# Kernel optimization log

Hardware: AMD Instinct MI355X
Metric: run time of the kernel (lower is better)

## Reference

```python
import jax, jax.numpy as jnp
import numpy as np

N_NODES = 20000
N_EDGES = 320000
NUM_FEATURES = 128
HIDDEN = 128
NUM_CLASSES = 40
GRID_SIZE = 4
SPLINE_ORDER = 3
NB = GRID_SIZE + SPLINE_ORDER  # basis functions per input feature
_H = 2.0 / GRID_SIZE  # grid_range [-1, 1]
GRID = jnp.arange(-SPLINE_ORDER, GRID_SIZE + SPLINE_ORDER + 1, dtype=jnp.float32) * _H - 1.0


def b_splines(x):
    # x: (N, in) -> (N, in, NB) via Cox-de Boor recursion (efficient-KAN)
    xg = x[..., None]
    b = ((xg >= GRID[:-1]) & (xg < GRID[1:])).astype(x.dtype)
    for k in range(1, SPLINE_ORDER + 1):
        b = ((xg - GRID[: -(k + 1)]) / (GRID[k:-1] - GRID[: -(k + 1)]) * b[..., :-1]
             + (GRID[k + 1:] - xg) / (GRID[k + 1:] - GRID[1:-k]) * b[..., 1:])
    return b


def kan_linear(x, base_w, spline_w):
    # base branch: silu(x) @ W_base^T ; spline branch: contraction over (in, NB)
    base = jax.nn.silu(x) @ base_w.T
    spline = jnp.einsum('nik,oik->no', b_splines(x), spline_w)
    return base + spline


def gcn_conv(h, base_w, spline_w, bias, src_f, dst_f, norm):
    h = kan_linear(h, base_w, spline_w)
    msg = h[src_f] * norm[:, None]  # gather + edge scaling
    out = jax.ops.segment_sum(msg, dst_f, num_segments=N_NODES)
    return out + bias


def batchnorm(h, gamma, beta):
    mean = h.mean(axis=0)
    var = h.var(axis=0)  # biased, as torch BN uses for normalization
    return (h - mean) * jax.lax.rsqrt(var + 1e-5) * gamma + beta


def setup_inputs() -> dict:
    key = jax.random.key(0)
    ks = jax.random.split(key, 8)
    s = 0.1
    return {
        'x': jax.random.normal(ks[0], (N_NODES, NUM_FEATURES), dtype=jnp.float32),
        'edge_index': jax.random.randint(ks[1], (2, N_EDGES), 0, N_NODES, dtype=jnp.int64),
        'base_w0': jax.random.normal(ks[2], (HIDDEN, NUM_FEATURES), dtype=jnp.float32) * s,
        'spline_w0': jax.random.normal(ks[3], (HIDDEN, NUM_FEATURES, NB), dtype=jnp.float32) * s,
        'bias0': jnp.zeros((HIDDEN,), dtype=jnp.float32),
        'base_w1': jax.random.normal(ks[4], (HIDDEN, HIDDEN), dtype=jnp.float32) * s,
        'spline_w1': jax.random.normal(ks[5], (HIDDEN, HIDDEN, NB), dtype=jnp.float32) * s,
        'bias1': jnp.zeros((HIDDEN,), dtype=jnp.float32),
        'base_w_out': jax.random.normal(ks[6], (NUM_CLASSES, NUM_FEATURES + 2 * HIDDEN), dtype=jnp.float32) * s,
        'spline_w_out': jax.random.normal(ks[7], (NUM_CLASSES, NUM_FEATURES + 2 * HIDDEN, NB), dtype=jnp.float32) * s,
        'bias_out': jnp.zeros((NUM_CLASSES,), dtype=jnp.float32),
        'gamma': jnp.ones((HIDDEN,), dtype=jnp.float32),
        'beta': jnp.zeros((HIDDEN,), dtype=jnp.float32),
    }


def reference(x, edge_index, base_w0, spline_w0, bias0, base_w1, spline_w1, bias1,
              base_w_out, spline_w_out, bias_out, gamma, beta):
    # gcn_norm with self loops (computed once, reused by every layer)
    loop = jnp.arange(N_NODES, dtype=edge_index.dtype)
    src_f = jnp.concatenate([edge_index[0], loop])
    dst_f = jnp.concatenate([edge_index[1], loop])
    deg = jax.ops.segment_sum(jnp.ones_like(dst_f, dtype=x.dtype), dst_f, num_segments=N_NODES)
    dinv = jnp.where(deg > 0, jax.lax.rsqrt(jnp.maximum(deg, 1e-12)), 0.0)
    norm = dinv[src_f] * dinv[dst_f]

    skips = [x]
    h = x
    for bw, sw, b in ((base_w0, spline_w0, bias0), (base_w1, spline_w1, bias1)):
        h = gcn_conv(h, bw, sw, b, src_f, dst_f, norm)
        h = batchnorm(h, gamma, beta)  # shared BN, dropout p=0.0 is identity
        skips.append(h)
    h = jnp.concatenate(skips, axis=1)  # (N, 128 + 2*128)
    return gcn_conv(h, base_w_out, spline_w_out, bias_out, src_f, dst_f, norm)
```

## Files before the change

kernel.cpp:

```cpp
#include <hip/hip_runtime.h>

#define NN 20000

typedef _Float16 half8 __attribute__((ext_vector_type(8)));
typedef _Float16 half2v __attribute__((ext_vector_type(2)));
typedef float floatx16 __attribute__((ext_vector_type(16)));

#define MFMA32(a, b, c) __builtin_amdgcn_mfma_f32_32x32x16_f16((a), (b), (c), 0, 0, 0)
#define LD8(p) (*(const half8*)(p))

__device__ __forceinline__ void gl_lds16(const _Float16* g, _Float16* l) {
  __builtin_amdgcn_global_load_lds((const __attribute__((address_space(1))) char*)g,
                                   (__attribute__((address_space(3))) char*)l, 16, 0, 0);
}

__device__ __forceinline__ void bspline7_fast(float x, float b[7]) {
  float u = (x + 2.5f) * 2.0f;
  float cf = floorf(u);
  int c = (int)cf;
  float t = u - cf;
  float omt = 1.0f - t;
  float t2 = t * t, t3 = t2 * t;
  float w0 = omt * omt * omt * (1.0f / 6.0f);
  float w1 = (3.0f * t3 - 6.0f * t2 + 4.0f) * (1.0f / 6.0f);
  float w2 = (-3.0f * t3 + 3.0f * t2 + 3.0f * t + 1.0f) * (1.0f / 6.0f);
  float w3 = t3 * (1.0f / 6.0f);
  bool valid = (c >= 0) && (c <= 9);
#pragma unroll
  for (int i = 0; i < 7; ++i) {
    int d = c - i;
    float w = (d == 0) ? w3 : (d == 1) ? w2 : (d == 2) ? w1 : (d == 3) ? w0 : 0.0f;
    b[i] = valid ? w : 0.0f;
  }
}

__device__ __forceinline__ float silu_f(float x) {
  return x * (1.0f / (1.0f + __expf(-x)));
}

__device__ __forceinline__ half8 afrag(float xv) {
  float b[7];
  bspline7_fast(xv, b);
  half8 hv;
  hv[0] = (_Float16)silu_f(xv);
#pragma unroll
  for (int k = 0; k < 7; ++k) hv[k + 1] = (_Float16)b[k];
  return hv;
}

__global__ void fb_kernel(const float* __restrict__ X, const float* __restrict__ ss,
                          _Float16* __restrict__ F) {
  int idx = blockIdx.x * 256 + threadIdx.x;
  if (idx >= NN * 128) return;
  int n = idx >> 7, i = idx & 127;
  float xv = X[idx] * ss[i] + ss[128 + i];
  *(half8*)(F + ((size_t)n * 128 + (i ^ (n & 7))) * 8) = afrag(xv);
}

__global__ void packw_all(const float* __restrict__ Wb0, const float* __restrict__ Ws0,
                          const float* __restrict__ Wb1, const float* __restrict__ Ws1,
                          const float* __restrict__ WbO, const float* __restrict__ WsO,
                          _Float16* __restrict__ WPA0, _Float16* __restrict__ WPA1,
                          _Float16* __restrict__ WPC) {
  int bid = blockIdx.x;
  if (bid < 1536) {
    int s = (bid >= 768) ? 1 : 0;
    int idx = (bid - s * 768) * 256 + threadIdx.x;
    if (idx >= 196608) return;
    const float* Wb = s ? Wb1 : Wb0;
    const float* Wsp = s ? Ws1 : Ws0;
    _Float16* WP = s ? WPA1 : WPA0;
    int j = idx & 7;
    int lane = (idx >> 3) & 63;
    int u = idx >> 9;
    int cb = u % 6, ks = u / 6;
    int i = ks * 2 + (lane >> 5);
    int o32 = lane & 31;
    float v = 0.0f;
    if (cb < 4) {
      int o = cb * 32 + o32;
      v = (j == 0) ? Wb[(size_t)o * 128 + i] : Wsp[(size_t)o * 896 + i * 7 + (j - 1)];
    } else {
      int o = (cb - 4) * 32 + o32;
      if (o < 40)
        v = (j == 0) ? WbO[(size_t)o * 384 + s * 128 + i]
                     : WsO[(size_t)o * 2688 + s * 896 + i * 7 + (j - 1)];
    }
    WP[idx] = (_Float16)v;
  } else {
    int idx = (bid - 1536) * 256 + threadIdx.x;
    if (idx >= 65536) return;
    int j = idx & 7;
    int lane = (idx >> 3) & 63;
    int u = idx >> 9;
    int cb = u & 1, ks = u >> 1;
    int i = ks * 2 + (lane >> 5);
    int o = cb * 32 + (lane & 31);
    float v = 0.0f;
    if (o < 40)
      v = (j == 0) ? WbO[(size_t)o * 384 + 2 * 128 + i]
                   : WsO[(size_t)o * 2688 + 2 * 896 + i * 7 + (j - 1)];
    WPC[idx] = (_Float16)v;
  }
}

__global__ void count_deg(const int* __restrict__ dst, int* __restrict__ degE, int E) {
  int e = blockIdx.x * 256 + threadIdx.x;
  if (e < E) atomicAdd(&degE[dst[e]], 1);
}

__global__ void build_meta2(const int* __restrict__ degE, int* __restrict__ rowptr,
                            int* __restrict__ cursor, float* __restrict__ dinv,
                            float* __restrict__ ssb, int n) {
  __shared__ int wsum[16];
  int tid = threadIdx.x, lane = tid & 63, wid = tid >> 6;
  if (tid < 256) ssb[tid] = (tid < 128) ? 1.0f : 0.0f;
  int i0 = tid * 20;
  int d[20];
  int s = 0;
#pragma unroll
  for (int j = 0; j < 20; ++j) {
    int i = i0 + j;
    int v = (i < n) ? degE[i] : 0;
    d[j] = v;
    s += v;
    if (i < n) dinv[i] = rsqrtf((float)(v + 1));
  }
  int val = s;
#pragma unroll
  for (int off = 1; off < 64; off <<= 1) {
    int t = __shfl_up(val, off);
    if (lane >= off) val += t;
  }
  if (lane == 63) wsum[wid] = val;
  __syncthreads();
  if (wid == 0) {
    int wv = (lane < 16) ? wsum[lane] : 0;
#pragma unroll
    for (int off = 1; off < 16; off <<= 1) {
      int t = __shfl_up(wv, off);
      if (lane >= off) wv += t;
    }
    if (lane < 16) wsum[lane] = wv;
  }
  __syncthreads();
  int base = (wid ? wsum[wid - 1] : 0) + val - s;
  if (tid == 0) rowptr[0] = 0;
#pragma unroll
  for (int j = 0; j < 20; ++j) {
    int i = i0 + j;
    if (i < n) {
      cursor[i] = base;
      rowptr[i + 1] = base + d[j];
      base += d[j];
    }
  }
}

__global__ void fill_csr(const int* __restrict__ src, const int* __restrict__ dst,
                         int* __restrict__ cursor, int* __restrict__ csr, int E) {
  int e = blockIdx.x * 256 + threadIdx.x;
  if (e < E) {
    int p = atomicAdd(&cursor[dst[e]], 1);
    csr[p] = src[e];
  }
}

__global__ __launch_bounds__(384) void gemmTA(const _Float16* __restrict__ Fg,
                                              const _Float16* __restrict__ WP,
                                              const float* __restrict__ dinv,
                                              _Float16* __restrict__ A, float* __restrict__ P) {
  __shared__ _Float16 Fs[32 * 1024];
  int tid = threadIdx.x;
  int lane = tid & 63, w = tid >> 6;
  int row0 = blockIdx.x * 32;
  const _Float16* Ft = Fg + (size_t)row0 * 1024;
  for (int i = w; i < 64; i += 6) gl_lds16(Ft + (size_t)i * 512 + lane * 8, Fs + (size_t)i * 512);
  __syncthreads();

  int r = lane & 31, hi = lane >> 5, rx = r & 7;
  const _Float16* Fr = Fs + (size_t)r * 1024;
  const _Float16* Bp = WP + ((size_t)w * 64 + lane) * 8;
  floatx16 acc = {};
#pragma unroll 4
  for (int ks = 0; ks < 64; ++ks) {
    half8 a = LD8(Fr + (size_t)((2 * ks + hi) ^ rx) * 8);
    half8 b = LD8(Bp + (size_t)ks * 3072);
    acc = MFMA32(a, b, acc);
  }
  int col = lane & 31;
  if (w < 4) {
#pragma unroll
    for (int q = 0; q < 16; ++q) {
      int rl = (q & 3) + 8 * (q >> 2) + 4 * hi;
      A[(size_t)(row0 + rl) * 128 + w * 32 + col] = (_Float16)(acc[q] * dinv[row0 + rl]);
    }
  } else {
#pragma unroll
    for (int q = 0; q < 16; ++q) {
      int rl = (q & 3) + 8 * (q >> 2) + 4 * hi;
      P[(size_t)(row0 + rl) * 64 + (w - 4) * 32 + col] = acc[q];
    }
  }
}

__global__ __launch_bounds__(256) void gemmTC(const _Float16* __restrict__ Fg,
                                              const _Float16* __restrict__ WP,
                                              const float* __restrict__ P0,
                                              const float* __restrict__ P1,
                                              const float* __restrict__ dinv,
                                              _Float16* __restrict__ C) {
  __shared__ _Float16 Fs[32 * 1024];
  int tid = threadIdx.x;
  int lane = tid & 63, w = tid >> 6;
  int cb = w & 1, kh = w >> 1;
  int row0 = blockIdx.x * 32;
  const _Float16* Ft = Fg + (size_t)row0 * 1024;
  for (int i = w; i < 64; i += 4) gl_lds16(Ft + (size_t)i * 512 + lane * 8, Fs + (size_t)i * 512);
  __syncthreads();

  int r = lane & 31, hi = lane >> 5, rx = r & 7;
  const _Float16* Fr = Fs + (size_t)r * 1024;
  const _Float16* Bp = WP + ((size_t)cb * 64 + lane) * 8;
  floatx16 acc = {};
  int ks0 = kh * 32;
#pragma unroll 4
  for (int ks = ks0; ks < ks0 + 32; ++ks) {
    half8 a = LD8(Fr + (size_t)((2 * ks + hi) ^ rx) * 8);
    half8 b = LD8(Bp + (size_t)ks * 1024);
    acc = MFMA32(a, b, acc);
  }
  __syncthreads();
  float* red = (float*)Fs;
  if (kh == 1) {
#pragma unroll
    for (int q = 0; q < 16; ++q) red[((size_t)cb * 64 + lane) * 16 + q] = acc[q];
  }
  __syncthreads();
  if (kh == 0) {
    int col = lane & 31;
#pragma unroll
    for (int q = 0; q < 16; ++q) {
      float v = acc[q] + red[((size_t)cb * 64 + lane) * 16 + q];
      int rl = (q & 3) + 8 * (q >> 2) + 4 * hi;
      size_t idx = (size_t)(row0 + rl) * 64 + cb * 32 + col;
      C[idx] = (_Float16)((v + P0[idx] + P1[idx]) * dinv[row0 + rl]);
    }
  }
}

__global__ __launch_bounds__(256) void aggregate128h(const _Float16* __restrict__ Ah,
                                                     const int* __restrict__ rowptr,
                                                     const int* __restrict__ csr,
                                                     const float* __restrict__ dinv,
                                                     const float* __restrict__ bias,
                                                     float* __restrict__ Y) {
  int wid = threadIdx.x >> 6, lane = threadIdx.x & 63;
  int n = blockIdx.x * 4 + wid;
  float di = dinv[n];
  half2v self = *(const half2v*)(Ah + (size_t)n * 128 + lane * 2);
  float a0 = (float)self[0], a1 = (float)self[1];
  float b0x = 0, b0y = 0, b1x = 0, b1y = 0, b2x = 0, b2y = 0, b3x = 0, b3y = 0;
  int e0 = rowptr[n], m = rowptr[n + 1] - e0;
  int j = 0;
  for (; j + 4 <= m; j += 4) {
    int s0 = csr[e0 + j], s1 = csr[e0 + j + 1], s2 = csr[e0 + j + 2], s3 = csr[e0 + j + 3];
    half2v r0 = *(const half2v*)(Ah + (size_t)s0 * 128 + lane * 2);
    half2v r1 = *(const half2v*)(Ah + (size_t)s1 * 128 + lane * 2);
    half2v r2 = *(const half2v*)(Ah + (size_t)s2 * 128 + lane * 2);
    half2v r3 = *(const half2v*)(Ah + (size_t)s3 * 128 + lane * 2);
    b0x += (float)r0[0]; b0y += (float)r0[1];
    b1x += (float)r1[0]; b1y += (float)r1[1];
    b2x += (float)r2[0]; b2y += (float)r2[1];
    b3x += (float)r3[0]; b3y += (float)r3[1];
  }
  for (; j < m; ++j) {
    int s = csr[e0 + j];
    half2v rr = *(const half2v*)(Ah + (size_t)s * 128 + lane * 2);
    b0x += (float)rr[0]; b0y += (float)rr[1];
  }
  a0 += (b0x + b1x) + (b2x + b3x);
  a1 += (b0y + b1y) + (b2y + b3y);
  float2 outv = {a0 * di + bias[lane * 2], a1 * di + bias[lane * 2 + 1]};
  *(float2*)(Y + (size_t)n * 128 + lane * 2) = outv;
}

__global__ __launch_bounds__(256) void aggregate40h(const _Float16* __restrict__ Ch,
                                                    const int* __restrict__ rowptr,
                                                    const int* __restrict__ csr,
                                                    const float* __restrict__ dinv,
                                                    const float* __restrict__ bias,
                                                    float* __restrict__ out) {
  int wid = threadIdx.x >> 6, lane = threadIdx.x & 63;
  int n = blockIdx.x * 4 + wid;
  float di = dinv[n];
  float a = (float)Ch[(size_t)n * 64 + lane];
  float b0 = 0, b1 = 0, b2 = 0, b3 = 0;
  int e0 = rowptr[n], m = rowptr[n + 1] - e0;
  int j = 0;
  for (; j + 4 <= m; j += 4) {
    int s0 = csr[e0 + j], s1 = csr[e0 + j + 1], s2 = csr[e0 + j + 2], s3 = csr[e0 + j + 3];
    b0 += (float)Ch[(size_t)s0 * 64 + lane];
    b1 += (float)Ch[(size_t)s1 * 64 + lane];
    b2 += (float)Ch[(size_t)s2 * 64 + lane];
    b3 += (float)Ch[(size_t)s3 * 64 + lane];
  }
  for (; j < m; ++j) {
    int s = csr[e0 + j];
    b0 += (float)Ch[(size_t)s * 64 + lane];
  }
  a += (b0 + b1) + (b2 + b3);
  if (lane < 40) out[(size_t)n * 40 + lane] = a * di + bias[lane];
}

__global__ __launch_bounds__(256) void bn_stats(const float* __restrict__ H,
                                                float* __restrict__ partial) {
  int tid = threadIdx.x;
  int c4 = (tid & 31) * 4;
  int r0 = blockIdx.x * 32 + (tid >> 5) * 4;
  float s0 = 0, s1 = 0, s2 = 0, s3 = 0, q0 = 0, q1 = 0, q2 = 0, q3 = 0;
#pragma unroll
  for (int j = 0; j < 4; ++j) {
    float4 v = *(const float4*)(H + (size_t)(r0 + j) * 128 + c4);
    s0 += v.x; s1 += v.y; s2 += v.z; s3 += v.w;
    q0 += v.x * v.x; q1 += v.y * v.y; q2 += v.z * v.z; q3 += v.w * v.w;
  }
  __shared__ float sh[2][256][4];
  sh[0][tid][0] = s0; sh[0][tid][1] = s1; sh[0][tid][2] = s2; sh[0][tid][3] = s3;
  sh[1][tid][0] = q0; sh[1][tid][1] = q1; sh[1][tid][2] = q2; sh[1][tid][3] = q3;
  __syncthreads();
  if (tid < 32) {
    float a0 = 0, a1 = 0, a2 = 0, a3 = 0, b0 = 0, b1 = 0, b2 = 0, b3 = 0;
#pragma unroll
    for (int g = 0; g < 8; ++g) {
      int u = g * 32 + tid;
      a0 += sh[0][u][0]; a1 += sh[0][u][1]; a2 += sh[0][u][2]; a3 += sh[0][u][3];
      b0 += sh[1][u][0]; b1 += sh[1][u][1]; b2 += sh[1][u][2]; b3 += sh[1][u][3];
    }
    float* p = partial + (size_t)blockIdx.x * 256;
    p[tid * 4 + 0] = a0; p[tid * 4 + 1] = a1; p[tid * 4 + 2] = a2; p[tid * 4 + 3] = a3;
    p[128 + tid * 4 + 0] = b0; p[128 + tid * 4 + 1] = b1;
    p[128 + tid * 4 + 2] = b2; p[128 + tid * 4 + 3] = b3;
  }
}

__global__ __launch_bounds__(256) void bn_reduce(const float* __restrict__ partial,
                                                 float* __restrict__ p2) {
  int tid = threadIdx.x;
  const float* base = partial + (size_t)blockIdx.x * 25 * 256 + tid;
  float a0 = 0, a1 = 0, a2 = 0, a3 = 0, a4 = 0;
#pragma unroll
  for (int j = 0; j < 5; ++j) {
    a0 += base[(j * 5 + 0) * 256];
    a1 += base[(j * 5 + 1) * 256];
    a2 += base[(j * 5 + 2) * 256];
    a3 += base[(j * 5 + 3) * 256];
    a4 += base[(j * 5 + 4) * 256];
  }
  p2[(size_t)blockIdx.x * 256 + tid] = ((a0 + a1) + (a2 + a3)) + a4;
}

__global__ __launch_bounds__(256) void bn_final2(const float* __restrict__ p2,
                                                 const float* __restrict__ gamma,
                                                 const float* __restrict__ beta,
                                                 float* __restrict__ ss) {
  int tid = threadIdx.x;
  double a0 = 0, a1 = 0, a2 = 0, a3 = 0, a4 = 0;
#pragma unroll
  for (int j = 0; j < 5; ++j) {
    a0 += (double)p2[(size_t)(j * 5 + 0) * 256 + tid];
    a1 += (double)p2[(size_t)(j * 5 + 1) * 256 + tid];
    a2 += (double)p2[(size_t)(j * 5 + 2) * 256 + tid];
    a3 += (double)p2[(size_t)(j * 5 + 3) * 256 + tid];
    a4 += (double)p2[(size_t)(j * 5 + 4) * 256 + tid];
  }
  double tot = ((a0 + a1) + (a2 + a3)) + a4;
  __shared__ double sh[256];
  sh[tid] = tot;
  __syncthreads();
  if (tid < 128) {
    double S = sh[tid];
    double Q = sh[128 + tid];
    double mean = S / (double)NN;
    double var = Q / (double)NN - mean * mean;
    float sc = gamma[tid] * rsqrtf((float)var + 1e-5f);
    ss[tid] = sc;
    ss[128 + tid] = beta[tid] - (float)mean * sc;
  }
}

extern "C" void kernel_launch(void* const* d_in, const int* in_sizes, int n_in,
                              void* d_out, int out_size, void* d_ws, size_t ws_size,
                              hipStream_t stream) {
  const float* x = (const float*)d_in[0];
  const int* ei = (const int*)d_in[1];
  const float* bw0 = (const float*)d_in[2];
  const float* sw0 = (const float*)d_in[3];
  const float* b0 = (const float*)d_in[4];
  const float* bw1 = (const float*)d_in[5];
  const float* sw1 = (const float*)d_in[6];
  const float* b1 = (const float*)d_in[7];
  const float* bwo = (const float*)d_in[8];
  const float* swo = (const float*)d_in[9];
  const float* bo = (const float*)d_in[10];
  const float* gamma = (const float*)d_in[11];
  const float* beta = (const float*)d_in[12];
  const int E = in_sizes[1] / 2;
  const int* esrc = ei;
  const int* edst = ei + E;

  char* ws = (char*)d_ws;
  size_t off = 0;
  auto alloc = [&](size_t bytes) -> void* {
    void* p = ws + off;
    off = (off + bytes + 255) & ~(size_t)255;
    return p;
  };
  _Float16* WPA0 = (_Float16*)alloc(196608 * 2);
  _Float16* WPA1 = (_Float16*)alloc(196608 * 2);
  _Float16* WPC = (_Float16*)alloc(65536 * 2);
  float* dinv = (float*)alloc(NN * 4);
  int* degE = (int*)alloc(NN * 4);
  int* rowptr = (int*)alloc((NN + 1) * 4);
  int* cursor = (int*)alloc(NN * 4);
  int* csr = (int*)alloc((size_t)E * 4);
  _Float16* Fg = (_Float16*)alloc((size_t)NN * 1024 * 2);
  _Float16* A = (_Float16*)alloc((size_t)NN * 128 * 2);
  float* h1 = (float*)alloc((size_t)NN * 128 * 4);
  float* P0 = (float*)alloc((size_t)NN * 64 * 4);
  float* P1 = (float*)alloc((size_t)NN * 64 * 4);
  _Float16* Ch = (_Float16*)alloc((size_t)NN * 64 * 2);
  float* partial = (float*)alloc((size_t)625 * 256 * 4);
  float* p2 = (float*)alloc((size_t)25 * 256 * 4);
  float* ssb = (float*)alloc(256 * 4);
  float* h2 = h1;
  (void)ws_size; (void)n_in; (void)out_size;

  int egrid = (E + 255) / 256;
  const int GG = 625;

  hipMemsetAsync(degE, 0, NN * sizeof(int), stream);
  packw_all<<<1792, 256, 0, stream>>>(bw0, sw0, bw1, sw1, bwo, swo, WPA0, WPA1, WPC);
  count_deg<<<egrid, 256, 0, stream>>>(edst, degE, E);
  build_meta2<<<1, 1024, 0, stream>>>(degE, rowptr, cursor, dinv, ssb, NN);
  fill_csr<<<egrid, 256, 0, stream>>>(esrc, edst, cursor, csr, E);

  fb_kernel<<<10000, 256, 0, stream>>>(x, ssb, Fg);
  gemmTA<<<GG, 384, 0, stream>>>(Fg, WPA0, dinv, A, P0);
  aggregate128h<<<5000, 256, 0, stream>>>(A, rowptr, csr, dinv, b0, h1);
  bn_stats<<<625, 256, 0, stream>>>(h1, partial);
  bn_reduce<<<25, 256, 0, stream>>>(partial, p2);
  bn_final2<<<1, 256, 0, stream>>>(p2, gamma, beta, ssb);

  fb_kernel<<<10000, 256, 0, stream>>>(h1, ssb, Fg);
  gemmTA<<<GG, 384, 0, stream>>>(Fg, WPA1, dinv, A, P1);
  aggregate128h<<<5000, 256, 0, stream>>>(A, rowptr, csr, dinv, b1, h2);
  bn_stats<<<625, 256, 0, stream>>>(h2, partial);
  bn_reduce<<<25, 256, 0, stream>>>(partial, p2);
  bn_final2<<<1, 256, 0, stream>>>(p2, gamma, beta, ssb);

  fb_kernel<<<10000, 256, 0, stream>>>(h2, ssb, Fg);
  gemmTC<<<GG, 256, 0, stream>>>(Fg, WPC, P0, P1, dinv, Ch);
  aggregate40h<<<5000, 256, 0, stream>>>(Ch, rowptr, csr, dinv, bo, (float*)d_out);
}
```

Baseline: 271.8 us.

## Fuse BatchNorm statistics into aggregation and collapse BN reduction kernels

```diff
diff --git a/kernel.cpp b/kernel.cpp
--- a/kernel.cpp
+++ b/kernel.cpp
@@ -61,7 +61,8 @@
                           const float* __restrict__ Wb1, const float* __restrict__ Ws1,
                           const float* __restrict__ WbO, const float* __restrict__ WsO,
                           _Float16* __restrict__ WPA0, _Float16* __restrict__ WPA1,
-                          _Float16* __restrict__ WPC) {
+                          _Float16* __restrict__ WPC, int* __restrict__ degE,
+                          float* __restrict__ ssb, float* __restrict__ partial) {
   int bid = blockIdx.x;
   if (bid < 1536) {
     int s = (bid >= 768) ? 1 : 0;
@@ -87,7 +88,7 @@
                      : WsO[(size_t)o * 2688 + s * 896 + i * 7 + (j - 1)];
     }
     WP[idx] = (_Float16)v;
-  } else {
+  } else if (bid < 1792) {
     int idx = (bid - 1536) * 256 + threadIdx.x;
     if (idx >= 65536) return;
     int j = idx & 7;
@@ -101,6 +102,14 @@
       v = (j == 0) ? WbO[(size_t)o * 384 + 2 * 128 + i]
                    : WsO[(size_t)o * 2688 + 2 * 896 + i * 7 + (j - 1)];
     WPC[idx] = (_Float16)v;
+  } else if (bid < 1871) {
+    int idx = (bid - 1792) * 256 + threadIdx.x;
+    if (idx < NN) degE[idx] = 0;
+  } else {
+    int t = threadIdx.x;
+    ssb[t] = (t < 128) ? 1.0f : 0.0f;
+    partial[1250 * 256 + t] = 0.0f;
+    partial[1250 * 256 + 256 + t] = 0.0f;
   }
 }
 
@@ -110,11 +119,9 @@
 }
 
 __global__ void build_meta2(const int* __restrict__ degE, int* __restrict__ rowptr,
-                            int* __restrict__ cursor, float* __restrict__ dinv,
-                            float* __restrict__ ssb, int n) {
+                            int* __restrict__ cursor, float* __restrict__ dinv, int n) {
   __shared__ int wsum[16];
   int tid = threadIdx.x, lane = tid & 63, wid = tid >> 6;
-  if (tid < 256) ssb[tid] = (tid < 128) ? 1.0f : 0.0f;
   int i0 = tid * 20;
   int d[20];
   int s = 0;
@@ -249,40 +256,105 @@
   }
 }
 
-__global__ __launch_bounds__(256) void aggregate128h(const _Float16* __restrict__ Ah,
-                                                     const int* __restrict__ rowptr,
-                                                     const int* __restrict__ csr,
-                                                     const float* __restrict__ dinv,
-                                                     const float* __restrict__ bias,
-                                                     float* __restrict__ Y) {
-  int wid = threadIdx.x >> 6, lane = threadIdx.x & 63;
-  int n = blockIdx.x * 4 + wid;
+__global__ __launch_bounds__(1024) void aggregate128hs(const _Float16* __restrict__ Ah,
+                                                       const int* __restrict__ rowptr,
+                                                       const int* __restrict__ csr,
+                                                       const float* __restrict__ dinv,
+                                                       const float* __restrict__ bias,
+                                                       float* __restrict__ Y,
+                                                       float* __restrict__ partial) {
+  int tid = threadIdx.x;
+  int wid = tid >> 6, lane = tid & 63;
+  int n = blockIdx.x * 16 + wid;
   float di = dinv[n];
   half2v self = *(const half2v*)(Ah + (size_t)n * 128 + lane * 2);
   float a0 = (float)self[0], a1 = (float)self[1];
-  float b0x = 0, b0y = 0, b1x = 0, b1y = 0, b2x = 0, b2y = 0, b3x = 0, b3y = 0;
+  float bx[8] = {0, 0, 0, 0, 0, 0, 0, 0}, by[8] = {0, 0, 0, 0, 0, 0, 0, 0};
   int e0 = rowptr[n], m = rowptr[n + 1] - e0;
   int j = 0;
-  for (; j + 4 <= m; j += 4) {
-    int s0 = csr[e0 + j], s1 = csr[e0 + j + 1], s2 = csr[e0 + j + 2], s3 = csr[e0 + j + 3];
-    half2v r0 = *(const half2v*)(Ah + (size_t)s0 * 128 + lane * 2);
-    half2v r1 = *(const half2v*)(Ah + (size_t)s1 * 128 + lane * 2);
-    half2v r2 = *(const half2v*)(Ah + (size_t)s2 * 128 + lane * 2);
-    half2v r3 = *(const half2v*)(Ah + (size_t)s3 * 128 + lane * 2);
-    b0x += (float)r0[0]; b0y += (float)r0[1];
-    b1x += (float)r1[0]; b1y += (float)r1[1];
-    b2x += (float)r2[0]; b2y += (float)r2[1];
-    b3x += (float)r3[0]; b3y += (float)r3[1];
+  for (; j + 8 <= m; j += 8) {
+    int s[8];
+#pragma unroll
+    for (int q = 0; q < 8; ++q) s[q] = csr[e0 + j + q];
+#pragma unroll
+    for (int q = 0; q < 8; ++q) {
+      half2v r = *(const half2v*)(Ah + (size_t)s[q] * 128 + lane * 2);
+      bx[q] += (float)r[0];
+      by[q] += (float)r[1];
+    }
   }
   for (; j < m; ++j) {
     int s = csr[e0 + j];
-    half2v rr = *(const half2v*)(Ah + (size_t)s * 128 + lane * 2);
-    b0x += (float)rr[0]; b0y += (float)rr[1];
-  }
-  a0 += (b0x + b1x) + (b2x + b3x);
-  a1 += (b0y + b1y) + (b2y + b3y);
-  float2 outv = {a0 * di + bias[lane * 2], a1 * di + bias[lane * 2 + 1]};
+    half2v r = *(const half2v*)(Ah + (size_t)s * 128 + lane * 2);
+    bx[0] += (float)r[0];
+    by[0] += (float)r[1];
+  }
+  a0 += ((bx[0] + bx[1]) + (bx[2] + bx[3])) + ((bx[4] + bx[5]) + (bx[6] + bx[7]));
+  a1 += ((by[0] + by[1]) + (by[2] + by[3])) + ((by[4] + by[5]) + (by[6] + by[7]));
+  float o0 = a0 * di + bias[lane * 2];
+  float o1 = a1 * di + bias[lane * 2 + 1];
+  float2 outv = {o0, o1};
   *(float2*)(Y + (size_t)n * 128 + lane * 2) = outv;
+
+  __shared__ float shA[16][128];
+  shA[wid][lane * 2] = o0;
+  shA[wid][lane * 2 + 1] = o1;
+  __syncthreads();
+  if (tid < 128) {
+    float s = 0;
+#pragma unroll
+    for (int w2 = 0; w2 < 16; ++w2) s += shA[w2][tid];
+    partial[(size_t)blockIdx.x * 256 + tid] = s;
+  }
+  __syncthreads();
+  shA[wid][lane * 2] = o0 * o0;
+  shA[wid][lane * 2 + 1] = o1 * o1;
+  __syncthreads();
+  if (tid < 128) {
+    float s = 0;
+#pragma unroll
+    for (int w2 = 0; w2 < 16; ++w2) s += shA[w2][tid];
+    partial[(size_t)blockIdx.x * 256 + 128 + tid] = s;
+  }
+}
+
+__global__ __launch_bounds__(1024) void bn_finalB(const float* __restrict__ partial,
+                                                  const float* __restrict__ gamma,
+                                                  const float* __restrict__ beta,
+                                                  float* __restrict__ ss) {
+  int tid = threadIdx.x;
+  int col = tid & 255, rg = tid >> 8;
+  const float* base = partial + (size_t)rg * 256 + col;
+  double a0 = 0, a1 = 0, a2 = 0, a3 = 0, a4 = 0;
+  for (int jj = 0; jj < 62; ++jj) {
+    size_t t = (size_t)jj * 5;
+    a0 += (double)base[(t + 0) * 1024];
+    a1 += (double)base[(t + 1) * 1024];
+    a2 += (double)base[(t + 2) * 1024];
+    a3 += (double)base[(t + 3) * 1024];
+    a4 += (double)base[(t + 4) * 1024];
+  }
+  a0 += (double)base[(size_t)310 * 1024];
+  a1 += (double)base[(size_t)311 * 1024];
+  a2 += (double)base[(size_t)312 * 1024];
+  double tot = ((a0 + a1) + (a2 + a3)) + a4;
+  __shared__ double shd[4][256];
+  shd[rg][col] = tot;
+  __syncthreads();
+  if (tid < 256) {
+    double S = (shd[0][tid] + shd[1][tid]) + (shd[2][tid] + shd[3][tid]);
+    shd[0][tid] = S;
+  }
+  __syncthreads();
+  if (tid < 128) {
+    double S = shd[0][tid];
+    double Q = shd[0][128 + tid];
+    double mean = S / (double)NN;
+    double var = Q / (double)NN - mean * mean;
+    float sc = gamma[tid] * rsqrtf((float)var + 1e-5f);
+    ss[tid] = sc;
+    ss[128 + tid] = beta[tid] - (float)mean * sc;
+  }
 }
 
 __global__ __launch_bounds__(256) void aggregate40h(const _Float16* __restrict__ Ch,
@@ -311,82 +383,6 @@
   }
   a += (b0 + b1) + (b2 + b3);
   if (lane < 40) out[(size_t)n * 40 + lane] = a * di + bias[lane];
-}
-
-__global__ __launch_bounds__(256) void bn_stats(const float* __restrict__ H,
-                                                float* __restrict__ partial) {
-  int tid = threadIdx.x;
-  int c4 = (tid & 31) * 4;
-  int r0 = blockIdx.x * 32 + (tid >> 5) * 4;
-  float s0 = 0, s1 = 0, s2 = 0, s3 = 0, q0 = 0, q1 = 0, q2 = 0, q3 = 0;
-#pragma unroll
-  for (int j = 0; j < 4; ++j) {
-    float4 v = *(const float4*)(H + (size_t)(r0 + j) * 128 + c4);
-    s0 += v.x; s1 += v.y; s2 += v.z; s3 += v.w;
-    q0 += v.x * v.x; q1 += v.y * v.y; q2 += v.z * v.z; q3 += v.w * v.w;
-  }
-  __shared__ float sh[2][256][4];
-  sh[0][tid][0] = s0; sh[0][tid][1] = s1; sh[0][tid][2] = s2; sh[0][tid][3] = s3;
-  sh[1][tid][0] = q0; sh[1][tid][1] = q1; sh[1][tid][2] = q2; sh[1][tid][3] = q3;
-  __syncthreads();
-  if (tid < 32) {
-    float a0 = 0, a1 = 0, a2 = 0, a3 = 0, b0 = 0, b1 = 0, b2 = 0, b3 = 0;
-#pragma unroll
-    for (int g = 0; g < 8; ++g) {
-      int u = g * 32 + tid;
-      a0 += sh[0][u][0]; a1 += sh[0][u][1]; a2 += sh[0][u][2]; a3 += sh[0][u][3];
-      b0 += sh[1][u][0]; b1 += sh[1][u][1]; b2 += sh[1][u][2]; b3 += sh[1][u][3];
-    }
-    float* p = partial + (size_t)blockIdx.x * 256;
-    p[tid * 4 + 0] = a0; p[tid * 4 + 1] = a1; p[tid * 4 + 2] = a2; p[tid * 4 + 3] = a3;
-    p[128 + tid * 4 + 0] = b0; p[128 + tid * 4 + 1] = b1;
-    p[128 + tid * 4 + 2] = b2; p[128 + tid * 4 + 3] = b3;
-  }
-}
-
-__global__ __launch_bounds__(256) void bn_reduce(const float* __restrict__ partial,
-                                                 float* __restrict__ p2) {
-  int tid = threadIdx.x;
-  const float* base = partial + (size_t)blockIdx.x * 25 * 256 + tid;
-  float a0 = 0, a1 = 0, a2 = 0, a3 = 0, a4 = 0;
-#pragma unroll
-  for (int j = 0; j < 5; ++j) {
-    a0 += base[(j * 5 + 0) * 256];
-    a1 += base[(j * 5 + 1) * 256];
-    a2 += base[(j * 5 + 2) * 256];
-    a3 += base[(j * 5 + 3) * 256];
-    a4 += base[(j * 5 + 4) * 256];
-  }
-  p2[(size_t)blockIdx.x * 256 + tid] = ((a0 + a1) + (a2 + a3)) + a4;
-}
-
-__global__ __launch_bounds__(256) void bn_final2(const float* __restrict__ p2,
-                                                 const float* __restrict__ gamma,
-                                                 const float* __restrict__ beta,
-                                                 float* __restrict__ ss) {
-  int tid = threadIdx.x;
-  double a0 = 0, a1 = 0, a2 = 0, a3 = 0, a4 = 0;
-#pragma unroll
-  for (int j = 0; j < 5; ++j) {
-    a0 += (double)p2[(size_t)(j * 5 + 0) * 256 + tid];
-    a1 += (double)p2[(size_t)(j * 5 + 1) * 256 + tid];
-    a2 += (double)p2[(size_t)(j * 5 + 2) * 256 + tid];
-    a3 += (double)p2[(size_t)(j * 5 + 3) * 256 + tid];
-    a4 += (double)p2[(size_t)(j * 5 + 4) * 256 + tid];
-  }
-  double tot = ((a0 + a1) + (a2 + a3)) + a4;
-  __shared__ double sh[256];
-  sh[tid] = tot;
-  __syncthreads();
-  if (tid < 128) {
-    double S = sh[tid];
-    double Q = sh[128 + tid];
-    double mean = S / (double)NN;
-    double var = Q / (double)NN - mean * mean;
-    float sc = gamma[tid] * rsqrtf((float)var + 1e-5f);
-    ss[tid] = sc;
-    ss[128 + tid] = beta[tid] - (float)mean * sc;
-  }
 }
 
 extern "C" void kernel_launch(void* const* d_in, const int* in_sizes, int n_in,
@@ -430,8 +426,7 @@
   float* P0 = (float*)alloc((size_t)NN * 64 * 4);
   float* P1 = (float*)alloc((size_t)NN * 64 * 4);
   _Float16* Ch = (_Float16*)alloc((size_t)NN * 64 * 2);
-  float* partial = (float*)alloc((size_t)625 * 256 * 4);
-  float* p2 = (float*)alloc((size_t)25 * 256 * 4);
+  float* partial = (float*)alloc((size_t)1252 * 256 * 4);
   float* ssb = (float*)alloc(256 * 4);
   float* h2 = h1;
   (void)ws_size; (void)n_in; (void)out_size;
@@ -439,25 +434,21 @@
   int egrid = (E + 255) / 256;
   const int GG = 625;
 
-  hipMemsetAsync(degE, 0, NN * sizeof(int), stream);
-  packw_all<<<1792, 256, 0, stream>>>(bw0, sw0, bw1, sw1, bwo, swo, WPA0, WPA1, WPC);
+  packw_all<<<1872, 256, 0, stream>>>(bw0, sw0, bw1, sw1, bwo, swo, WPA0, WPA1, WPC,
+                                      degE, ssb, partial);
   count_deg<<<egrid, 256, 0, stream>>>(edst, degE, E);
-  build_meta2<<<1, 1024, 0, stream>>>(degE, rowptr, cursor, dinv, ssb, NN);
+  build_meta2<<<1, 1024, 0, stream>>>(degE, rowptr, cursor, dinv, NN);
   fill_csr<<<egrid, 256, 0, stream>>>(esrc, edst, cursor, csr, E);
 
   fb_kernel<<<10000, 256, 0, stream>>>(x, ssb, Fg);
   gemmTA<<<GG, 384, 0, stream>>>(Fg, WPA0, dinv, A, P0);
-  aggregate128h<<<5000, 256, 0, stream>>>(A, rowptr, csr, dinv, b0, h1);
-  bn_stats<<<625, 256, 0, stream>>>(h1, partial);
-  bn_reduce<<<25, 256, 0, stream>>>(partial, p2);
-  bn_final2<<<1, 256, 0, stream>>>(p2, gamma, beta, ssb);
+  aggregate128hs<<<1250, 1024, 0, stream>>>(A, rowptr, csr, dinv, b0, h1, partial);
+  bn_finalB<<<1, 1024, 0, stream>>>(partial, gamma, beta, ssb);
 
   fb_kernel<<<10000, 256, 0, stream>>>(h1, ssb, Fg);
   gemmTA<<<GG, 384, 0, stream>>>(Fg, WPA1, dinv, A, P1);
-  aggregate128h<<<5000, 256, 0, stream>>>(A, rowptr, csr, dinv, b1, h2);
-  bn_stats<<<625, 256, 0, stream>>>(h2, partial);
-  bn_reduce<<<25, 256, 0, stream>>>(partial, p2);
-  bn_final2<<<1, 256, 0, stream>>>(p2, gamma, beta, ssb);
+  aggregate128hs<<<1250, 1024, 0, stream>>>(A, rowptr, csr, dinv, b1, h2, partial);
+  bn_finalB<<<1, 1024, 0, stream>>>(partial, gamma, beta, ssb);
 
   fb_kernel<<<10000, 256, 0, stream>>>(h2, ssb, Fg);
   gemmTC<<<GG, 256, 0, stream>>>(Fg, WPC, P0, P1, dinv, Ch);
```

After: 293.3 us. 7.9% more time.

## Fuse B-spline feature expansion into GEMM kernels and split K across more waves

Applied to the files above, without the earlier changes.

```diff
diff --git a/kernel.cpp b/kernel.cpp
--- a/kernel.cpp
+++ b/kernel.cpp
@@ -8,11 +8,6 @@
 
 #define MFMA32(a, b, c) __builtin_amdgcn_mfma_f32_32x32x16_f16((a), (b), (c), 0, 0, 0)
 #define LD8(p) (*(const half8*)(p))
-
-__device__ __forceinline__ void gl_lds16(const _Float16* g, _Float16* l) {
-  __builtin_amdgcn_global_load_lds((const __attribute__((address_space(1))) char*)g,
-                                   (__attribute__((address_space(3))) char*)l, 16, 0, 0);
-}
 
 __device__ __forceinline__ void bspline7_fast(float x, float b[7]) {
   float u = (x + 2.5f) * 2.0f;
@@ -48,20 +43,12 @@
   return hv;
 }
 
-__global__ void fb_kernel(const float* __restrict__ X, const float* __restrict__ ss,
-                          _Float16* __restrict__ F) {
-  int idx = blockIdx.x * 256 + threadIdx.x;
-  if (idx >= NN * 128) return;
-  int n = idx >> 7, i = idx & 127;
-  float xv = X[idx] * ss[i] + ss[128 + i];
-  *(half8*)(F + ((size_t)n * 128 + (i ^ (n & 7))) * 8) = afrag(xv);
-}
-
 __global__ void packw_all(const float* __restrict__ Wb0, const float* __restrict__ Ws0,
                           const float* __restrict__ Wb1, const float* __restrict__ Ws1,
                           const float* __restrict__ WbO, const float* __restrict__ WsO,
                           _Float16* __restrict__ WPA0, _Float16* __restrict__ WPA1,
-                          _Float16* __restrict__ WPC) {
+                          _Float16* __restrict__ WPC, int* __restrict__ degE,
+                          float* __restrict__ ssb) {
   int bid = blockIdx.x;
   if (bid < 1536) {
     int s = (bid >= 768) ? 1 : 0;
@@ -87,7 +74,7 @@
                      : WsO[(size_t)o * 2688 + s * 896 + i * 7 + (j - 1)];
     }
     WP[idx] = (_Float16)v;
-  } else {
+  } else if (bid < 1792) {
     int idx = (bid - 1536) * 256 + threadIdx.x;
     if (idx >= 65536) return;
     int j = idx & 7;
@@ -101,6 +88,12 @@
       v = (j == 0) ? WbO[(size_t)o * 384 + 2 * 128 + i]
                    : WsO[(size_t)o * 2688 + 2 * 896 + i * 7 + (j - 1)];
     WPC[idx] = (_Float16)v;
+  } else if (bid < 1871) {
+    int idx = (bid - 1792) * 256 + threadIdx.x;
+    if (idx < NN) degE[idx] = 0;
+  } else {
+    int t = threadIdx.x;
+    ssb[t] = (t < 128) ? 1.0f : 0.0f;
   }
 }
 
@@ -110,11 +103,9 @@
 }
 
 __global__ void build_meta2(const int* __restrict__ degE, int* __restrict__ rowptr,
-                            int* __restrict__ cursor, float* __restrict__ dinv,
-                            float* __restrict__ ssb, int n) {
+                            int* __restrict__ cursor, float* __restrict__ dinv, int n) {
   __shared__ int wsum[16];
   int tid = threadIdx.x, lane = tid & 63, wid = tid >> 6;
-  if (tid < 256) ssb[tid] = (tid < 128) ? 1.0f : 0.0f;
   int i0 = tid * 20;
   int d[20];
   int s = 0;
@@ -166,45 +157,57 @@
   }
 }
 
-__global__ __launch_bounds__(384) void gemmTA(const _Float16* __restrict__ Fg,
+__global__ __launch_bounds__(768) void gemmSA(const float* __restrict__ X,
+                                              const float* __restrict__ ss,
                                               const _Float16* __restrict__ WP,
                                               const float* __restrict__ dinv,
                                               _Float16* __restrict__ A, float* __restrict__ P) {
   __shared__ _Float16 Fs[32 * 1024];
   int tid = threadIdx.x;
   int lane = tid & 63, w = tid >> 6;
+  int cb = w % 6, kh = w / 6;
   int row0 = blockIdx.x * 32;
-  const _Float16* Ft = Fg + (size_t)row0 * 1024;
-  for (int i = w; i < 64; i += 6) gl_lds16(Ft + (size_t)i * 512 + lane * 8, Fs + (size_t)i * 512);
+  for (int idx = tid; idx < 4096; idx += 768) {
+    int r = idx >> 7, i = idx & 127;
+    float xv = X[(size_t)(row0 + r) * 128 + i] * ss[i] + ss[128 + i];
+    *(half8*)(Fs + ((size_t)r * 128 + (i ^ (r & 7))) * 8) = afrag(xv);
+  }
   __syncthreads();
 
   int r = lane & 31, hi = lane >> 5, rx = r & 7;
   const _Float16* Fr = Fs + (size_t)r * 1024;
-  const _Float16* Bp = WP + ((size_t)w * 64 + lane) * 8;
+  const _Float16* Bp = WP + ((size_t)cb * 64 + lane) * 8;
   floatx16 acc = {};
+  int ks0 = kh * 32;
 #pragma unroll 4
-  for (int ks = 0; ks < 64; ++ks) {
+  for (int ks = ks0; ks < ks0 + 32; ++ks) {
     half8 a = LD8(Fr + (size_t)((2 * ks + hi) ^ rx) * 8);
     half8 b = LD8(Bp + (size_t)ks * 3072);
     acc = MFMA32(a, b, acc);
   }
-  int col = lane & 31;
-  if (w < 4) {
+  __syncthreads();
+  float* red = (float*)Fs;
+  if (kh == 1) {
+#pragma unroll
+    for (int q = 0; q < 16; ++q) red[q * 384 + cb * 64 + lane] = acc[q];
+  }
+  __syncthreads();
+  if (kh == 0) {
+    int col = lane & 31;
 #pragma unroll
     for (int q = 0; q < 16; ++q) {
+      float v = acc[q] + red[q * 384 + cb * 64 + lane];
       int rl = (q & 3) + 8 * (q >> 2) + 4 * hi;
-      A[(size_t)(row0 + rl) * 128 + w * 32 + col] = (_Float16)(acc[q] * dinv[row0 + rl]);
-    }
-  } else {
-#pragma unroll
-    for (int q = 0; q < 16; ++q) {
-      int rl = (q & 3) + 8 * (q >> 2) + 4 * hi;
-      P[(size_t)(row0 + rl) * 64 + (w - 4) * 32 + col] = acc[q];
-    }
-  }
-}
-
-__global__ __launch_bounds__(256) void gemmTC(const _Float16* __restrict__ Fg,
+      if (cb < 4)
+        A[(size_t)(row0 + rl) * 128 + cb * 32 + col] = (_Float16)(v * dinv[row0 + rl]);
+      else
+        P[(size_t)(row0 + rl) * 64 + (cb - 4) * 32 + col] = v;
+    }
+  }
+}
+
+__global__ __launch_bounds__(512) void gemmSC(const float* __restrict__ X,
+                                              const float* __restrict__ ss,
                                               const _Float16* __restrict__ WP,
                                               const float* __restrict__ P0,
                                               const float* __restrict__ P1,
@@ -215,33 +218,38 @@
   int lane = tid & 63, w = tid >> 6;
   int cb = w & 1, kh = w >> 1;
   int row0 = blockIdx.x * 32;
-  const _Float16* Ft = Fg + (size_t)row0 * 1024;
-  for (int i = w; i < 64; i += 4) gl_lds16(Ft + (size_t)i * 512 + lane * 8, Fs + (size_t)i * 512);
+  for (int idx = tid; idx < 4096; idx += 512) {
+    int r = idx >> 7, i = idx & 127;
+    float xv = X[(size_t)(row0 + r) * 128 + i] * ss[i] + ss[128 + i];
+    *(half8*)(Fs + ((size_t)r * 128 + (i ^ (r & 7))) * 8) = afrag(xv);
+  }
   __syncthreads();
 
   int r = lane & 31, hi = lane >> 5, rx = r & 7;
   const _Float16* Fr = Fs + (size_t)r * 1024;
   const _Float16* Bp = WP + ((size_t)cb * 64 + lane) * 8;
   floatx16 acc = {};
-  int ks0 = kh * 32;
+  int ks0 = kh * 16;
 #pragma unroll 4
-  for (int ks = ks0; ks < ks0 + 32; ++ks) {
+  for (int ks = ks0; ks < ks0 + 16; ++ks) {
     half8 a = LD8(Fr + (size_t)((2 * ks + hi) ^ rx) * 8);
     half8 b = LD8(Bp + (size_t)ks * 1024);
     acc = MFMA32(a, b, acc);
   }
   __syncthreads();
   float* red = (float*)Fs;
-  if (kh == 1) {
-#pragma unroll
-    for (int q = 0; q < 16; ++q) red[((size_t)cb * 64 + lane) * 16 + q] = acc[q];
+  if (kh > 0) {
+#pragma unroll
+    for (int q = 0; q < 16; ++q)
+      red[((kh - 1) * 16 + q) * 128 + cb * 64 + lane] = acc[q];
   }
   __syncthreads();
   if (kh == 0) {
     int col = lane & 31;
 #pragma unroll
     for (int q = 0; q < 16; ++q) {
-      float v = acc[q] + red[((size_t)cb * 64 + lane) * 16 + q];
+      float v = acc[q] + red[q * 128 + cb * 64 + lane] +
+                red[(16 + q) * 128 + cb * 64 + lane] + red[(32 + q) * 128 + cb * 64 + lane];
       int rl = (q & 3) + 8 * (q >> 2) + 4 * hi;
       size_t idx = (size_t)(row0 + rl) * 64 + cb * 32 + col;
       C[idx] = (_Float16)((v + P0[idx] + P1[idx]) * dinv[row0 + rl]);
@@ -424,7 +432,6 @@
   int* rowptr = (int*)alloc((NN + 1) * 4);
   int* cursor = (int*)alloc(NN * 4);
   int* csr = (int*)alloc((size_t)E * 4);
-  _Float16* Fg = (_Float16*)alloc((size_t)NN * 1024 * 2);
   _Float16* A = (_Float16*)alloc((size_t)NN * 128 * 2);
   float* h1 = (float*)alloc((size_t)NN * 128 * 4);
   float* P0 = (float*)alloc((size_t)NN * 64 * 4);
@@ -439,27 +446,24 @@
   int egrid = (E + 255) / 256;
   const int GG = 625;
 
-  hipMemsetAsync(degE, 0, NN * sizeof(int), stream);
-  packw_all<<<1792, 256, 0, stream>>>(bw0, sw0, bw1, sw1, bwo, swo, WPA0, WPA1, WPC);
+  packw_all<<<1872, 256, 0, stream>>>(bw0, sw0, bw1, sw1, bwo, swo, WPA0, WPA1, WPC,
+                                      degE, ssb);
   count_deg<<<egrid, 256, 0, stream>>>(edst, degE, E);
-  build_meta2<<<1, 1024, 0, stream>>>(degE, rowptr, cursor, dinv, ssb, NN);
+  build_meta2<<<1, 1024, 0, stream>>>(degE, rowptr, cursor, dinv, NN);
   fill_csr<<<egrid, 256, 0, stream>>>(esrc, edst, cursor, csr, E);
 
-  fb_kernel<<<10000, 256, 0, stream>>>(x, ssb, Fg);
-  gemmTA<<<GG, 384, 0, stream>>>(Fg, WPA0, dinv, A, P0);
+  gemmSA<<<GG, 768, 0, stream>>>(x, ssb, WPA0, dinv, A, P0);
   aggregate128h<<<5000, 256, 0, stream>>>(A, rowptr, csr, dinv, b0, h1);
   bn_stats<<<625, 256, 0, stream>>>(h1, partial);
   bn_reduce<<<25, 256, 0, stream>>>(partial, p2);
   bn_final2<<<1, 256, 0, stream>>>(p2, gamma, beta, ssb);
 
-  fb_kernel<<<10000, 256, 0, stream>>>(h1, ssb, Fg);
-  gemmTA<<<GG, 384, 0, stream>>>(Fg, WPA1, dinv, A, P1);
+  gemmSA<<<GG, 768, 0, stream>>>(h1, ssb, WPA1, dinv, A, P1);
   aggregate128h<<<5000, 256, 0, stream>>>(A, rowptr, csr, dinv, b1, h2);
   bn_stats<<<625, 256, 0, stream>>>(h2, partial);
   bn_reduce<<<25, 256, 0, stream>>>(partial, p2);
   bn_final2<<<1, 256, 0, stream>>>(p2, gamma, beta, ssb);
 
-  fb_kernel<<<10000, 256, 0, stream>>>(h2, ssb, Fg);
-  gemmTC<<<GG, 256, 0, stream>>>(Fg, WPC, P0, P1, dinv, Ch);
+  gemmSC<<<GG, 512, 0, stream>>>(h2, ssb, WPC, P0, P1, dinv, Ch);
   aggregate40h<<<5000, 256, 0, stream>>>(Ch, rowptr, csr, dinv, bo, (float*)d_out);
 }
```

Measured after the change: 240.3 us (median of 2 runs). -11.6%, faster.
